# Performance work log

Hardware: AMD Instinct MI355X
Metric: run time of the kernel (lower is better)

The kernel has to match this reference:

```python
import jax, jax.numpy as jnp
import numpy as np

PROJ_EPS = 4e-3      # geoopt-style Poincare projection margin (float32)
MIN_NORM = 1e-15
ATANH_EPS = 1e-5     # clamp arg of arctanh away from 1
WEI_EPS = 1e-3       # self.eps buffer
P_EXP = 2.0          # self.p buffer


def _project(v, k):
    # Project onto Poincare ball of curvature -k: clip norm to (1-eps)/sqrt(k).
    # k has shape (1,H,1,1), v has shape (B,H,T,D).
    maxnorm = (1.0 - PROJ_EPS) / jnp.sqrt(k)
    norm = jnp.sqrt(jnp.clip(jnp.sum(v * v, axis=-1, keepdims=True), MIN_NORM))
    return jnp.where(norm > maxnorm, v / norm * maxnorm, v)


def setup_inputs() -> dict:
    key = jax.random.key(0)
    k1, k2, k3, k4 = jax.random.split(key, 4)
    B, T, C, H = 4, 1024, 768, 12
    x = jax.random.normal(k1, (B, T, C), dtype=jnp.float32)
    Wqkv = jax.random.normal(k2, (3 * C, C), dtype=jnp.float32) * (1.0 / np.sqrt(C))
    Wproj = jax.random.normal(k3, (C, C), dtype=jnp.float32) * (1.0 / np.sqrt(C))
    # learnable per-head curvature, init ~ exp(randn)*curvature (must be > 0)
    kcurv = jax.random.uniform(k4, (1, H, 1, 1), dtype=jnp.float32, minval=0.5, maxval=1.5)
    return {"x": x, "Wqkv": Wqkv, "Wproj": Wproj, "kcurv": kcurv}


def reference(x, Wqkv, Wproj, kcurv):
    B, T, C = x.shape
    H = kcurv.shape[1]
    D = C // H

    qkv = x @ Wqkv.T                                  # (B,T,3C)
    q, kx, v = jnp.split(qkv, 3, axis=-1)

    def to_heads(t):
        return t.reshape(B, T, H, D).transpose(0, 2, 1, 3)  # (B,H,T,D)

    q, kx, v = to_heads(q), to_heads(kx), to_heads(v)

    qp = _project(q, kcurv)
    kp = _project(kx, kcurv)

    # Poincare distance d(x,y) = (2/sqrt(k)) * artanh(sqrt(k)*||(-x) mobius+ y||).
    # mobius_add(-x,y) = (-(1-2k<x,y>+k|y|^2) x + (1-k|x|^2) y) / (1-2k<x,y>+k^2|x|^2|y|^2)
    # => ||num||^2 = A^2|x|^2 + Bc^2|y|^2 - 2*A*Bc*<x,y>, avoiding (B,H,T,T,D) tensors.
    x2 = jnp.sum(qp * qp, axis=-1)                    # (B,H,T)
    y2 = jnp.sum(kp * kp, axis=-1)                    # (B,H,T)
    xy = jnp.einsum('bhid,bhjd->bhij', qp, kp)        # (B,H,T,T)

    kc = kcurv                                        # (1,H,1,1) broadcasts to (B,H,T,T)
    x2i = x2[..., :, None]                            # (B,H,T,1)
    y2j = y2[..., None, :]                            # (B,H,1,T)

    A = 1.0 - 2.0 * kc * xy + kc * y2j
    Bc = 1.0 - kc * x2i
    num2 = A * A * x2i + Bc * Bc * y2j - 2.0 * A * Bc * xy
    denom = 1.0 - 2.0 * kc * xy + (kc * kc) * x2i * y2j
    madd_norm = jnp.sqrt(jnp.clip(num2, MIN_NORM)) / jnp.clip(denom, MIN_NORM)

    sk = jnp.sqrt(kc)
    dist = (2.0 / sk) * jnp.arctanh(jnp.clip(sk * madd_norm, 0.0, 1.0 - ATANH_EPS))

    wei = 1.0 / (WEI_EPS + dist ** P_EXP)             # (B,H,T,T)
    causal = jnp.tril(jnp.ones((T, T), dtype=bool))
    wei = jnp.where(causal, wei, 0.0)
    wei = wei / jnp.sum(wei, axis=-1, keepdims=True)

    y = jnp.einsum('bhij,bhjd->bhid', wei, v)         # (B,H,T,D)
    y = y.transpose(0, 2, 1, 3).reshape(B, T, C)
    return y @ Wproj.T
```

## Files before the change

kernel.cpp:

```cpp
#include <hip/hip_runtime.h>
#include <hip/hip_bf16.h>
#include <math.h>

#define PROJ_EPSF 0.004f
#define MIN_NORMF 1e-15f
#define ATANH_EPSF 1e-5f
#define WEI_EPSF 1e-3f
#define LN2F 0.69314718055994531f

#define TT 1024
#define CC 768
#define HH 12
#define BBATCH 4

typedef unsigned long long ull;
typedef __attribute__((ext_vector_type(4))) float f32x4;
typedef __attribute__((ext_vector_type(8))) short bf16x8;

#define MFMA(a, b, c) __builtin_amdgcn_mfma_f32_16x16x32_bf16(a, b, c, 0, 0, 0)

static __device__ __forceinline__ uint cvtpk(float a, float b) {
    uint r;
    asm("v_cvt_pk_bf16_f32 %0, %1, %2" : "=v"(r) : "v"(a), "v"(b));
    return r;
}
static __device__ __forceinline__ ushort f2bf(float f) {
    uint u = __float_as_uint(f);
    u += 0x7fffu + ((u >> 16) & 1u);
    return (ushort)(u >> 16);
}
static __device__ __forceinline__ float bf2f(ushort h) {
    return __uint_as_float(((uint)h) << 16);
}
static __device__ __forceinline__ void split4(const float4& f, ull& hp, ull& lp) {
    uint h01 = cvtpk(f.x, f.y), h23 = cvtpk(f.z, f.w);
    float r0 = f.x - __uint_as_float(h01 << 16);
    float r1 = f.y - __uint_as_float(h01 & 0xffff0000u);
    float r2 = f.z - __uint_as_float(h23 << 16);
    float r3 = f.w - __uint_as_float(h23 & 0xffff0000u);
    uint l01 = cvtpk(r0, r1), l23 = cvtpk(r2, r3);
    hp = ((ull)h23 << 32) | h01;
    lp = ((ull)l23 << 32) | l01;
}
union pk16 { bf16x8 v; ull u[2]; };
static __device__ __forceinline__ void gl_lds16(const void* g, void* l) {
    __builtin_amdgcn_global_load_lds(
        (const __attribute__((address_space(1))) unsigned int*)g,
        (__attribute__((address_space(3))) unsigned int*)l, 16, 0, 0);
}

__global__ __launch_bounds__(256) void wprep(const float* __restrict__ W,
                                             ushort* __restrict__ Wh,
                                             ushort* __restrict__ Wl, int n4) {
    int i = blockIdx.x * 256 + threadIdx.x;
    if (i < n4) {
        float4 f = ((const float4*)W)[i];
        ull hp, lp;
        split4(f, hp, lp);
        ((ull*)Wh)[i] = hp;
        ((ull*)Wl)[i] = lp;
    }
}

__global__ __launch_bounds__(256) void gemm_qkv(
        const float* __restrict__ x, const ushort* __restrict__ Wh,
        const ushort* __restrict__ Wl, const float* __restrict__ kcurv,
        ushort* __restrict__ qh, ushort* __restrict__ ql,
        ushort* __restrict__ kh, ushort* __restrict__ kl,
        ushort* __restrict__ vT, float* __restrict__ x2g,
        float* __restrict__ y2g) {
    __shared__ ushort Ah[64 * 64], Al[64 * 64], Bh[64 * 64], Bl[64 * 64];
    const int tid = threadIdx.x, lane = tid & 63, wv = tid >> 6;
    const int wr = wv >> 1, wc = wv & 1, lr = lane & 15, lg = lane >> 4;
    const int m0 = blockIdx.x * 128, n0 = blockIdx.y * 128;
    const bool isV = (n0 >= 2 * CC);

    const int arow = tid >> 1, akh = tid & 1;
    const float* Ap = x + (size_t)(m0 + arow) * CC + akh * 16;
    const int ap_ = arow >> 1;
    const int ag0 = 4 * (arow & 1) + 2 * akh;
    const int aoff0 = ap_ * 128 + ((ag0 ^ (ap_ & 7)) << 4);
    const int aoff1 = ap_ * 128 + (((ag0 + 1) ^ (ap_ & 7)) << 4);
    const int c0 = 2 * wv, c1 = 2 * wv + 1;
    const int p0 = 8 * c0 + (lane >> 3), q0 = (lane & 7) ^ (p0 & 7);
    const int p1 = 8 * c1 + (lane >> 3), q1 = (lane & 7) ^ (p1 & 7);
    const size_t bs0 = (size_t)(n0 + 2 * p0 + (q0 >> 2)) * CC + (q0 & 3) * 8;
    const size_t bs1 = (size_t)(n0 + 2 * p1 + (q1 >> 2)) * CC + (q1 & 3) * 8;
    const int goff = (((4 * (lr & 1) + lg) ^ ((lr >> 1) & 7)) << 4);
    const int pa = wr * 32 + (lr >> 1);
    const int pb = wc * 32 + (lr >> 1);

    f32x4 acc[4][4] = {};
    float4 av[4];
#pragma unroll
    for (int q = 0; q < 4; ++q) av[q] = *(const float4*)(Ap + 4 * q);

    for (int kk = 0; kk < CC; kk += 32) {
        __syncthreads();
        pk16 h, l;
        split4(av[0], h.u[0], l.u[0]);
        split4(av[1], h.u[1], l.u[1]);
        *(bf16x8*)((char*)Ah + aoff0) = h.v;
        if (!isV) *(bf16x8*)((char*)Al + aoff0) = l.v;
        split4(av[2], h.u[0], l.u[0]);
        split4(av[3], h.u[1], l.u[1]);
        *(bf16x8*)((char*)Ah + aoff1) = h.v;
        if (!isV) *(bf16x8*)((char*)Al + aoff1) = l.v;
        gl_lds16(Wh + bs0 + kk, (char*)Bh + c0 * 1024);
        gl_lds16(Wh + bs1 + kk, (char*)Bh + c1 * 1024);
        if (!isV) {
            gl_lds16(Wl + bs0 + kk, (char*)Bl + c0 * 1024);
            gl_lds16(Wl + bs1 + kk, (char*)Bl + c1 * 1024);
        }
        asm volatile("s_waitcnt vmcnt(0)" ::: "memory");
        __syncthreads();
        if (kk + 32 < CC)
#pragma unroll
            for (int q = 0; q < 4; ++q)
                av[q] = *(const float4*)(Ap + kk + 32 + 4 * q);
        if (!isV) {
            bf16x8 a_h[4], a_l[4];
#pragma unroll
            for (int m = 0; m < 4; ++m) {
                const int off = (pa + m * 8) * 128 + goff;
                a_h[m] = *(const bf16x8*)((char*)Ah + off);
                a_l[m] = *(const bf16x8*)((char*)Al + off);
            }
#pragma unroll
            for (int n = 0; n < 4; ++n) {
                const int off = (pb + n * 8) * 128 + goff;
                bf16x8 b_h = *(const bf16x8*)((char*)Bh + off);
                bf16x8 b_l = *(const bf16x8*)((char*)Bl + off);
#pragma unroll
                for (int m = 0; m < 4; ++m) {
                    acc[m][n] = MFMA(a_h[m], b_h, acc[m][n]);
                    acc[m][n] = MFMA(a_h[m], b_l, acc[m][n]);
                    acc[m][n] = MFMA(a_l[m], b_h, acc[m][n]);
                }
            }
        } else {
            bf16x8 a_h[4], b_h[4];
#pragma unroll
            for (int m = 0; m < 4; ++m)
                a_h[m] = *(const bf16x8*)((char*)Ah + (pa + m * 8) * 128 + goff);
#pragma unroll
            for (int n = 0; n < 4; ++n)
                b_h[n] = *(const bf16x8*)((char*)Bh + (pb + n * 8) * 128 + goff);
#pragma unroll
            for (int n = 0; n < 4; ++n)
#pragma unroll
                for (int m = 0; m < 4; ++m)
                    acc[n][m] = MFMA(b_h[n], a_h[m], acc[n][m]);
        }
    }
    if (isV) {
        const int hd = (n0 - 2 * CC) / 64 + wc;
#pragma unroll
        for (int n = 0; n < 4; ++n)
#pragma unroll
            for (int m = 0; m < 4; ++m)
#pragma unroll
                for (int r = 0; r < 4; ++r) {
                    const int dl = n * 16 + lg * 4 + r;
                    const int tok = m0 + wr * 64 + m * 16 + lr;
                    vT[(size_t)(hd * 64 + dl) * 4096 + tok] = f2bf(acc[n][m][r]);
                }
    } else {
        const bool isQ = (n0 < CC);
        const int hd = (isQ ? n0 : n0 - CC) / 64 + wc;
        ushort* ph = isQ ? qh : kh;
        ushort* pl = isQ ? ql : kl;
        float* sg = isQ ? x2g : y2g;
        const float kcv = kcurv[hd];
        const float mxn = (1.0f - PROJ_EPSF) / sqrtf(kcv);
        const float mxn2 = mxn * mxn;
#pragma unroll
        for (int m = 0; m < 4; ++m)
#pragma unroll
            for (int r = 0; r < 4; ++r) {
                float s = 0.f;
#pragma unroll
                for (int n = 0; n < 4; ++n) s = fmaf(acc[m][n][r], acc[m][n][r], s);
                s += __shfl_xor(s, 1);
                s += __shfl_xor(s, 2);
                s += __shfl_xor(s, 4);
                s += __shfl_xor(s, 8);
                float scale = 1.0f, x2v = s;
                if (s > mxn2) {
                    scale = mxn * __builtin_amdgcn_rcpf(sqrtf(s));
                    x2v = s * scale * scale;
                }
                const int tok = m0 + wr * 64 + m * 16 + lg * 4 + r;
                const size_t rowb = (size_t)tok * CC + (isQ ? n0 : n0 - CC) + wc * 64;
#pragma unroll
                for (int n = 0; n < 4; ++n) {
                    const float v = acc[m][n][r] * scale;
                    const ushort hb = f2bf(v);
                    ph[rowb + n * 16 + lr] = hb;
                    pl[rowb + n * 16 + lr] = f2bf(v - bf2f(hb));
                }
                if (lr == 0)
                    sg[(size_t)((tok >> 10) * HH + hd) * TT + (tok & 1023)] = x2v;
            }
    }
}

__global__ __launch_bounds__(256) void hyp_attn(
        const ushort* __restrict__ qh, const ushort* __restrict__ ql,
        const ushort* __restrict__ kh, const ushort* __restrict__ kl,
        const ushort* __restrict__ vT, const float* __restrict__ x2g,
        const float* __restrict__ y2g, const float* __restrict__ kcurv,
        ushort* __restrict__ yh, ushort* __restrict__ yl) {
    const int ib = (int)blockIdx.x;
    const int xcd = ib & 7, t = ib >> 3;
    const int tcr = t / 6;
    const int which = t - tcr * 6;
    const int g64 = 15 - tcr;
    const int bh = which * 8 + xcd;
    const int b = bh / HH, h = bh - b * HH;
    const int tid = threadIdx.x, lane = tid & 63, wv = tid >> 6;
    const int lr = lane & 15, lg = lane >> 4;
    const int rg = g64 * 4 + wv;
    const int rgq = g64;

    __shared__ char ldsK[2][16384];
    __shared__ char ldsV[8192];
    __shared__ ushort wtb[4][16 * 72];
    ushort* wtw = wtb[wv];

    const float kc = kcurv[h];
    const float sk = sqrtf(kc);
    const float distc = LN2F / sk;
    const float d2c = distc * distc;
    const float twokc = 2.0f * kc;
    const float cA = 1.0f - ATANH_EPSF;

    const size_t qrb = (size_t)(b * TT + rg * 16 + lr) * CC + h * 64 + lg * 8;
    const bf16x8 qH0 = *(const bf16x8*)(qh + qrb), qH1 = *(const bf16x8*)(qh + qrb + 32);
    const bf16x8 qL0 = *(const bf16x8*)(ql + qrb), qL1 = *(const bf16x8*)(ql + qrb + 32);
    const float4 x2v = *(const float4*)&x2g[(size_t)bh * TT + rg * 16 + lg * 4];
    const float x2a[4] = { x2v.x, x2v.y, x2v.z, x2v.w };
    float kx2[4], Bc[4], Bc2[4];
#pragma unroll
    for (int r = 0; r < 4; ++r) {
        kx2[r] = kc * x2a[r];
        Bc[r] = 1.0f - kx2[r];
        Bc2[r] = Bc[r] * Bc[r];
    }

    const int srow8 = lane >> 3;
    const int sgrp = (lane & 7) ^ (srow8 & 7);
    const int so0 = ((lg ^ (lr & 7)) << 4);
    const int so1 = (((4 + lg) ^ (lr & 7)) << 4);
    const int lro = lr << 7;

#define STAGE_K(BUF, J0)                                                          \
    { _Pragma("unroll") for (int c4 = 0; c4 < 2; ++c4) {                          \
        const int c = wv * 2 + c4;                                                \
        const size_t gsrc = (size_t)(b * TT + (J0) + c * 8 + srow8) * CC + h * 64 + sgrp * 8; \
        gl_lds16(kh + gsrc, (char*)(BUF) + c * 1024);                             \
        gl_lds16(kl + gsrc, (char*)(BUF) + 8192 + c * 1024);                      \
    } }
#define STAGE_V(J0)                                                               \
    { _Pragma("unroll") for (int c4 = 0; c4 < 2; ++c4) {                          \
        const int c = wv * 2 + c4;                                                \
        gl_lds16(vT + (size_t)(h * 64 + c * 8 + srow8) * 4096 + b * TT + (J0) + sgrp * 8, \
                 ldsV + c * 1024);                                                \
    } }

#define TRANSF(NN, SA, Y2R)                                                        \
    {                                                                              \
        const float ky2 = kc * (Y2R);                                              \
        const float p1 = 1.0f + ky2;                                               \
        const int jg = j0 + NN * 16 + lr;                                          \
        _Pragma("unroll") for (int r = 0; r < 4; ++r) {                            \
            const float xy = SA[r];                                                \
            const float t2 = twokc * xy;                                           \
            const float Aa = p1 - t2;                                              \
            const float dn = fmaxf(fmaf(kx2[r], ky2, 1.0f) - t2, MIN_NORMF);       \
            const float ABxy = Aa * (Bc[r] * xy);                                  \
            const float c1 = fmaf(Bc2[r], (Y2R), -2.0f * ABxy);                    \
            const float num2 = fmaf(Aa * Aa, x2a[r], c1);                          \
            const float s = sqrtf(fmaxf(num2, MIN_NORMF));                         \
            const float sm = fminf(sk * s, cA * dn);                               \
            const float L = __builtin_amdgcn_logf((dn + sm) *                      \
                                __builtin_amdgcn_rcpf(dn - sm));                   \
            float w = __builtin_amdgcn_rcpf(fmaf(L * L, d2c, WEI_EPSF));           \
            if (mk && (jg > rg * 16 + lg * 4 + r)) w = 0.0f;                       \
            wtw[(lg * 4 + r) * 72 + NN * 16 + lr] = f2bf(w);                       \
            wsum[r] += w;                                                          \
        }                                                                          \
    }

    f32x4 pv[4] = {};
    float wsum[4] = {};

    STAGE_K(ldsK[0], 0)

    int cur = 0;
    for (int jt = 0; jt <= rgq; ++jt) {
        const int j0 = jt * 64;
        const bool mk = (jt == rgq);
        STAGE_V(j0)
        if (jt < rgq) {
            STAGE_K(ldsK[cur ^ 1], j0 + 64)
            asm volatile("s_waitcnt vmcnt(6)" ::: "memory");
        } else {
            asm volatile("s_waitcnt vmcnt(2)" ::: "memory");
        }
        __builtin_amdgcn_s_barrier();
        __builtin_amdgcn_sched_barrier(0);
        const size_t y2b = (size_t)bh * TT + j0 + lr;
        const float y2n[4] = { y2g[y2b], y2g[y2b + 16], y2g[y2b + 32], y2g[y2b + 48] };
        __builtin_amdgcn_s_setprio(1);
        f32x4 sacc[4] = {};
#pragma unroll
        for (int n = 0; n < 4; ++n) {
            const char* p = ldsK[cur] + n * 2048 + lro;
            bf16x8 h0 = *(const bf16x8*)(p + so0);
            bf16x8 h1 = *(const bf16x8*)(p + so1);
            bf16x8 l0 = *(const bf16x8*)(p + 8192 + so0);
            bf16x8 l1 = *(const bf16x8*)(p + 8192 + so1);
            sacc[n] = MFMA(qH0, h0, sacc[n]);
            sacc[n] = MFMA(qH0, l0, sacc[n]);
            sacc[n] = MFMA(qL0, h0, sacc[n]);
            sacc[n] = MFMA(qH1, h1, sacc[n]);
            sacc[n] = MFMA(qH1, l1, sacc[n]);
            sacc[n] = MFMA(qL1, h1, sacc[n]);
        }
        TRANSF(0, sacc[0], y2n[0])
        TRANSF(1, sacc[1], y2n[1])
        TRANSF(2, sacc[2], y2n[2])
        TRANSF(3, sacc[3], y2n[3])
        __builtin_amdgcn_s_setprio(0);
        if (jt < rgq)
            asm volatile("s_waitcnt vmcnt(4)" ::: "memory");
        else
            asm volatile("s_waitcnt vmcnt(0)" ::: "memory");
        __builtin_amdgcn_s_barrier();
        __builtin_amdgcn_sched_barrier(0);
        __builtin_amdgcn_s_setprio(1);
        bf16x8 pw0 = *(const bf16x8*)&wtw[lr * 72 + lg * 8];
        bf16x8 pw1 = *(const bf16x8*)&wtw[lr * 72 + 32 + lg * 8];
#pragma unroll
        for (int n = 0; n < 4; ++n) {
            const char* p = ldsV + n * 2048 + lro;
            bf16x8 v0 = *(const bf16x8*)(p + so0);
            bf16x8 v1 = *(const bf16x8*)(p + so1);
            pv[n] = MFMA(pw0, v0, pv[n]);
            pv[n] = MFMA(pw1, v1, pv[n]);
        }
        __builtin_amdgcn_s_setprio(0);
        __builtin_amdgcn_s_barrier();
        cur ^= 1;
    }

    float den[4];
#pragma unroll
    for (int r = 0; r < 4; ++r) {
        float s = wsum[r];
        s += __shfl_xor(s, 1);
        s += __shfl_xor(s, 2);
        s += __shfl_xor(s, 4);
        s += __shfl_xor(s, 8);
        den[r] = s;
    }
#pragma unroll
    for (int r = 0; r < 4; ++r) {
        const float iv = __builtin_amdgcn_rcpf(den[r]);
        const size_t rowb = (size_t)(b * TT + rg * 16 + lg * 4 + r) * CC + h * 64;
#pragma unroll
        for (int n = 0; n < 4; ++n) {
            const float val = pv[n][r] * iv;
            const ushort hb = f2bf(val);
            yh[rowb + n * 16 + lr] = hb;
            yl[rowb + n * 16 + lr] = f2bf(val - bf2f(hb));
        }
    }
#undef TRANSF
#undef STAGE_K
#undef STAGE_V
}

__global__ __launch_bounds__(256) void gemm_out(const ushort* __restrict__ Ahp,
                                                const ushort* __restrict__ Alp,
                                                const ushort* __restrict__ Wh,
                                                const ushort* __restrict__ Wl,
                                                float* __restrict__ C) {
    __shared__ ushort Ah[2][32 * 64], Al[2][32 * 64], Bh[2][32 * 64], Bl[2][32 * 64];
    const int tid = threadIdx.x, lane = tid & 63, wv = tid >> 6;
    const int wr = wv >> 1, wc = wv & 1, lr = lane & 15, lg = lane >> 4;
    const int m0 = blockIdx.x * 64, n0 = blockIdx.y * 64;

    const int sp = 8 * wv + (lane >> 3);
    const int sg = (lane & 7) ^ (sp & 7);
    const int srow = 2 * sp + (sg >> 2);
    const int scol = (sg & 3) * 8;
    const size_t asrc = (size_t)(m0 + srow) * CC + scol;
    const size_t bsrc = (size_t)(n0 + srow) * CC + scol;
    const int goff = (((4 * (lr & 1) + lg) ^ ((lr >> 1) & 7)) << 4);
    const int pa = wr * 16 + (lr >> 1);
    const int pb = wc * 16 + (lr >> 1);

    f32x4 acc[2][2] = {};

#define STAGE_O(BUF, KK)                                                          \
    gl_lds16(Ahp + asrc + (KK), (char*)Ah[BUF] + wv * 1024);                      \
    gl_lds16(Alp + asrc + (KK), (char*)Al[BUF] + wv * 1024);                      \
    gl_lds16(Wh + bsrc + (KK), (char*)Bh[BUF] + wv * 1024);                       \
    gl_lds16(Wl + bsrc + (KK), (char*)Bl[BUF] + wv * 1024);

    STAGE_O(0, 0)
    int cur = 0;
    for (int kk = 0; kk < CC; kk += 32) {
        if (kk + 32 < CC) {
            STAGE_O(cur ^ 1, kk + 32)
            asm volatile("s_waitcnt vmcnt(4)" ::: "memory");
        } else {
            asm volatile("s_waitcnt vmcnt(0)" ::: "memory");
        }
        __builtin_amdgcn_s_barrier();
        __builtin_amdgcn_sched_barrier(0);
        bf16x8 a_h[2], a_l[2];
#pragma unroll
        for (int m = 0; m < 2; ++m) {
            const int off = (pa + m * 8) * 128 + goff;
            a_h[m] = *(const bf16x8*)((char*)Ah[cur] + off);
            a_l[m] = *(const bf16x8*)((char*)Al[cur] + off);
        }
#pragma unroll
        for (int n = 0; n < 2; ++n) {
            const int off = (pb + n * 8) * 128 + goff;
            bf16x8 b_h = *(const bf16x8*)((char*)Bh[cur] + off);
            bf16x8 b_l = *(const bf16x8*)((char*)Bl[cur] + off);
#pragma unroll
            for (int m = 0; m < 2; ++m) {
                acc[m][n] = MFMA(a_h[m], b_h, acc[m][n]);
                acc[m][n] = MFMA(a_h[m], b_l, acc[m][n]);
                acc[m][n] = MFMA(a_l[m], b_h, acc[m][n]);
            }
        }
        __builtin_amdgcn_s_barrier();
        cur ^= 1;
    }
#undef STAGE_O
#pragma unroll
    for (int m = 0; m < 2; ++m)
#pragma unroll
        for (int n = 0; n < 2; ++n)
#pragma unroll
            for (int r = 0; r < 4; ++r)
                C[(size_t)(m0 + wr * 32 + m * 16 + lg * 4 + r) * CC + n0 + wc * 32 + n * 16 + lr] =
                    acc[m][n][r];
}

extern "C" void kernel_launch(void* const* d_in, const int* in_sizes, int n_in,
                              void* d_out, int out_size, void* d_ws, size_t ws_size,
                              hipStream_t stream) {
    const float* x     = (const float*)d_in[0];
    const float* Wqkv  = (const float*)d_in[1];
    const float* Wproj = (const float*)d_in[2];
    const float* kcurv = (const float*)d_in[3];
    float* out = (float*)d_out;

    const size_t PL = (size_t)4096 * CC;
    char* w = (char*)d_ws;
    ushort* Wqh = (ushort*)w;
    ushort* Wql = Wqh + (size_t)2304 * CC;
    ushort* yh  = (ushort*)w;
    ushort* yl  = yh + PL;
    ushort* qh  = (ushort*)(w + 2 * PL * 2);
    ushort* ql  = qh + PL;
    ushort* kh  = ql + PL;
    ushort* kl  = kh + PL;
    ushort* vT  = kl + PL;
    ushort* Wph = vT + PL;
    ushort* Wpl = Wph + (size_t)CC * CC;
    float* x2g  = (float*)(Wpl + (size_t)CC * CC);
    float* y2g  = x2g + 48 * TT;

    wprep<<<2304 * CC / 4 / 256, 256, 0, stream>>>(Wqkv, Wqh, Wql, 2304 * CC / 4);
    wprep<<<CC * CC / 4 / 256, 256, 0, stream>>>(Wproj, Wph, Wpl, CC * CC / 4);
    gemm_qkv<<<dim3(32, 18), 256, 0, stream>>>(x, Wqh, Wql, kcurv,
                                               qh, ql, kh, kl, vT, x2g, y2g);
    hyp_attn<<<768, 256, 0, stream>>>(qh, ql, kh, kl, vT, x2g, y2g, kcurv, yh, yl);
    gemm_out<<<dim3(64, 12), 256, 0, stream>>>(yh, yl, Wph, Wpl, out);
}
```

Before: 143.3 us.

## Double-buffer LDS tiles in QKV GEMM to overlap loads with MFMA

Turns the QKV projection GEMM main loop into a two-stage software pipeline with ping-pong LDS buffers. The next tile's weight global-to-LDS copies and the split of the activation tile into bf16 hi/lo halves are issued before the current tile's MFMAs, and only one barrier is used per iteration. The goal is to hide global load latency behind compute. In exchange, LDS use doubles to 64KB per block, which can reduce occupancy, and correctness now depends on the manual vmcnt counts matching the number of outstanding loads.

```diff
diff --git a/kernel.cpp b/kernel.cpp
--- a/kernel.cpp
+++ b/kernel.cpp
@@ -69,7 +69,7 @@
         ushort* __restrict__ kh, ushort* __restrict__ kl,
         ushort* __restrict__ vT, float* __restrict__ x2g,
         float* __restrict__ y2g) {
-    __shared__ ushort Ah[64 * 64], Al[64 * 64], Bh[64 * 64], Bl[64 * 64];
+    __shared__ ushort Ah[2][64 * 64], Al[2][64 * 64], Bh[2][64 * 64], Bl[2][64 * 64];
     const int tid = threadIdx.x, lane = tid & 63, wv = tid >> 6;
     const int wr = wv >> 1, wc = wv & 1, lr = lane & 15, lg = lane >> 4;
     const int m0 = blockIdx.x * 128, n0 = blockIdx.y * 128;
@@ -92,45 +92,60 @@
 
     f32x4 acc[4][4] = {};
     float4 av[4];
-#pragma unroll
-    for (int q = 0; q < 4; ++q) av[q] = *(const float4*)(Ap + 4 * q);
-
+
+#define STAGE_B(BUF, KK)                                                          \
+    gl_lds16(Wh + bs0 + (KK), (char*)Bh[BUF] + c0 * 1024);                        \
+    gl_lds16(Wh + bs1 + (KK), (char*)Bh[BUF] + c1 * 1024);                        \
+    if (!isV) {                                                                   \
+        gl_lds16(Wl + bs0 + (KK), (char*)Bl[BUF] + c0 * 1024);                    \
+        gl_lds16(Wl + bs1 + (KK), (char*)Bl[BUF] + c1 * 1024);                    \
+    }
+#define SPLIT_A(BUF)                                                              \
+    {                                                                             \
+        pk16 h_, l_;                                                              \
+        split4(av[0], h_.u[0], l_.u[0]);                                          \
+        split4(av[1], h_.u[1], l_.u[1]);                                          \
+        *(bf16x8*)((char*)Ah[BUF] + aoff0) = h_.v;                                \
+        if (!isV) *(bf16x8*)((char*)Al[BUF] + aoff0) = l_.v;                      \
+        split4(av[2], h_.u[0], l_.u[0]);                                          \
+        split4(av[3], h_.u[1], l_.u[1]);                                          \
+        *(bf16x8*)((char*)Ah[BUF] + aoff1) = h_.v;                                \
+        if (!isV) *(bf16x8*)((char*)Al[BUF] + aoff1) = l_.v;                      \
+    }
+#define LOAD_A(KK)                                                                \
+    { _Pragma("unroll") for (int q = 0; q < 4; ++q)                               \
+        av[q] = *(const float4*)(Ap + (KK) + 4 * q); }
+
+    LOAD_A(0)
+    STAGE_B(0, 0)
+    SPLIT_A(0)
+    LOAD_A(32)
+    asm volatile("s_waitcnt vmcnt(4) lgkmcnt(0)" ::: "memory");
+    __builtin_amdgcn_s_barrier();
+    __builtin_amdgcn_sched_barrier(0);
+
+    int cur = 0;
     for (int kk = 0; kk < CC; kk += 32) {
-        __syncthreads();
-        pk16 h, l;
-        split4(av[0], h.u[0], l.u[0]);
-        split4(av[1], h.u[1], l.u[1]);
-        *(bf16x8*)((char*)Ah + aoff0) = h.v;
-        if (!isV) *(bf16x8*)((char*)Al + aoff0) = l.v;
-        split4(av[2], h.u[0], l.u[0]);
-        split4(av[3], h.u[1], l.u[1]);
-        *(bf16x8*)((char*)Ah + aoff1) = h.v;
-        if (!isV) *(bf16x8*)((char*)Al + aoff1) = l.v;
-        gl_lds16(Wh + bs0 + kk, (char*)Bh + c0 * 1024);
-        gl_lds16(Wh + bs1 + kk, (char*)Bh + c1 * 1024);
-        if (!isV) {
-            gl_lds16(Wl + bs0 + kk, (char*)Bl + c0 * 1024);
-            gl_lds16(Wl + bs1 + kk, (char*)Bl + c1 * 1024);
-        }
-        asm volatile("s_waitcnt vmcnt(0)" ::: "memory");
-        __syncthreads();
-        if (kk + 32 < CC)
-#pragma unroll
-            for (int q = 0; q < 4; ++q)
-                av[q] = *(const float4*)(Ap + kk + 32 + 4 * q);
+        const bool notLast = (kk + 32 < CC);
+        if (notLast) {
+            STAGE_B(cur ^ 1, kk + 32)
+            SPLIT_A(cur ^ 1)
+            if (kk + 64 < CC) LOAD_A(kk + 64)
+            __builtin_amdgcn_sched_barrier(0);
+        }
         if (!isV) {
             bf16x8 a_h[4], a_l[4];
 #pragma unroll
             for (int m = 0; m < 4; ++m) {
                 const int off = (pa + m * 8) * 128 + goff;
-                a_h[m] = *(const bf16x8*)((char*)Ah + off);
-                a_l[m] = *(const bf16x8*)((char*)Al + off);
+                a_h[m] = *(const bf16x8*)((char*)Ah[cur] + off);
+                a_l[m] = *(const bf16x8*)((char*)Al[cur] + off);
             }
 #pragma unroll
             for (int n = 0; n < 4; ++n) {
                 const int off = (pb + n * 8) * 128 + goff;
-                bf16x8 b_h = *(const bf16x8*)((char*)Bh + off);
-                bf16x8 b_l = *(const bf16x8*)((char*)Bl + off);
+                bf16x8 b_h = *(const bf16x8*)((char*)Bh[cur] + off);
+                bf16x8 b_l = *(const bf16x8*)((char*)Bl[cur] + off);
 #pragma unroll
                 for (int m = 0; m < 4; ++m) {
                     acc[m][n] = MFMA(a_h[m], b_h, acc[m][n]);
@@ -142,17 +157,30 @@
             bf16x8 a_h[4], b_h[4];
 #pragma unroll
             for (int m = 0; m < 4; ++m)
-                a_h[m] = *(const bf16x8*)((char*)Ah + (pa + m * 8) * 128 + goff);
+                a_h[m] = *(const bf16x8*)((char*)Ah[cur] + (pa + m * 8) * 128 + goff);
 #pragma unroll
             for (int n = 0; n < 4; ++n)
-                b_h[n] = *(const bf16x8*)((char*)Bh + (pb + n * 8) * 128 + goff);
+                b_h[n] = *(const bf16x8*)((char*)Bh[cur] + (pb + n * 8) * 128 + goff);
 #pragma unroll
             for (int n = 0; n < 4; ++n)
 #pragma unroll
                 for (int m = 0; m < 4; ++m)
                     acc[n][m] = MFMA(b_h[n], a_h[m], acc[n][m]);
         }
-    }
+        if (notLast) {
+            if (kk + 64 < CC)
+                asm volatile("s_waitcnt vmcnt(4) lgkmcnt(0)" ::: "memory");
+            else
+                asm volatile("s_waitcnt vmcnt(0) lgkmcnt(0)" ::: "memory");
+            __builtin_amdgcn_s_barrier();
+            __builtin_amdgcn_sched_barrier(0);
+        }
+        cur ^= 1;
+    }
+#undef STAGE_B
+#undef SPLIT_A
+#undef LOAD_A
+
     if (isV) {
         const int hd = (n0 - 2 * CC) / 64 + wc;
 #pragma unroll
```

Result: no change. 142.7 us (-0.4%).
